# Kernel optimization log

Measured on AMD Instinct MI355X. Metric: run time of the kernel, lower is better.

Reference implementation:

```python
import jax, jax.numpy as jnp
import numpy as np

DIM = 1024
N_HEADS = 16
HEAD_DIM = DIM // N_HEADS
B, N, M = 2, 2048, 2048


def setup_inputs() -> dict:
    key = jax.random.key(0)
    ks = jax.random.split(key, 10)
    s = 1.0 / np.sqrt(DIM)
    return {
        "x1": jax.random.normal(ks[0], (B, N, DIM), dtype=jnp.float32),
        "x2": jax.random.normal(ks[1], (B, M, DIM), dtype=jnp.float32),
        "Wq": jax.random.normal(ks[2], (DIM, DIM), dtype=jnp.float32) * s,
        "bq": jnp.zeros((DIM,), dtype=jnp.float32),
        "Wk": jax.random.normal(ks[3], (DIM, DIM), dtype=jnp.float32) * s,
        "bk": jnp.zeros((DIM,), dtype=jnp.float32),
        "Wv": jax.random.normal(ks[4], (DIM, DIM), dtype=jnp.float32) * s,
        "bv": jnp.zeros((DIM,), dtype=jnp.float32),
        "Wo": jax.random.normal(ks[5], (DIM, DIM), dtype=jnp.float32) * s,
        "bo": jnp.zeros((DIM,), dtype=jnp.float32),
    }


def reference(x1, x2, Wq, bq, Wk, bk, Wv, bv, Wo, bo):
    b, n, _ = x1.shape
    m = x2.shape[1]
    # projections (Linear: x @ W^T + b)
    q = x1 @ Wq.T + bq  # [b, n, dim]
    k = x2 @ Wk.T + bk  # [b, m, dim]
    v = x2 @ Wv.T + bv  # [b, m, dim]
    # split heads -> [b, h, seq, head_dim]
    q = q.reshape(b, n, N_HEADS, HEAD_DIM).transpose(0, 2, 1, 3)
    k = k.reshape(b, m, N_HEADS, HEAD_DIM).transpose(0, 2, 1, 3)
    v = v.reshape(b, m, N_HEADS, HEAD_DIM).transpose(0, 2, 1, 3)
    scale = 1.0 / jnp.sqrt(jnp.asarray(HEAD_DIM, dtype=q.dtype))
    scores = jnp.einsum('bhnd,bhmd->bhnm', q, k) * scale  # [b, h, n, m]
    attn = jax.nn.softmax(scores, axis=-1)
    o = jnp.einsum('bhnm,bhmd->bhnd', attn, v)  # [b, h, n, head_dim]
    o = o.transpose(0, 2, 1, 3).reshape(b, n, DIM)  # merge heads
    return o @ Wo.T + bo
```

## Files before the change

### kernel.cpp

```cpp
#include <hip/hip_runtime.h>
#include <stdint.h>

typedef unsigned short u16;
typedef __attribute__((ext_vector_type(4))) float f32x4;
typedef __attribute__((ext_vector_type(16))) float f32x16;
typedef __attribute__((ext_vector_type(8))) __bf16 bf16x8;
typedef __attribute__((ext_vector_type(8))) unsigned short u16x8;
typedef __attribute__((ext_vector_type(4))) unsigned short u16x4;

#define DIM_    1024
#define NHEADS_ 16
#define HD_     64
#define BB_     2
#define NN_     2048
#define MM_     2048

#define QSCALE 0.180336884f

__device__ inline u16 f32_to_bf16u(float f) {
  union { float f; uint32_t u; } x; x.f = f;
  uint32_t r = x.u + 0x7FFFu + ((x.u >> 16) & 1u);
  return (u16)(r >> 16);
}

__device__ inline void gload_lds16(const u16* g, u16* l) {
  u16* gnc = const_cast<u16*>(g);
  __builtin_amdgcn_global_load_lds(
      (__attribute__((address_space(1))) void*)gnc,
      (__attribute__((address_space(3))) void*)l, 16, 0, 0);
}

__device__ inline uint32_t cvt_pk_bf16(float lo, float hi) {
  uint32_t r;
  asm("v_cvt_pk_bf16_f32 %0, %1, %2" : "=v"(r) : "v"(lo), "v"(hi));
  return r;
}
__device__ inline void permlane32_swap(uint32_t& a, uint32_t& b) {
  asm("v_permlane32_swap_b32 %0, %1" : "+v"(a), "+v"(b));
}

__global__ void cast_all(const float* s0, u16* d0, const float* s1, u16* d1,
                         const float* s2, u16* d2, const float* s3, u16* d3,
                         const float* s4, u16* d4, const float* s5, u16* d5) {
  const float* s; u16* d; int n4;
  switch (blockIdx.y) {
    case 0: s = s0; d = d0; n4 = (BB_ * NN_ * DIM_) / 4; break;
    case 1: s = s1; d = d1; n4 = (BB_ * MM_ * DIM_) / 4; break;
    case 2: s = s2; d = d2; n4 = (DIM_ * DIM_) / 4; break;
    case 3: s = s3; d = d3; n4 = (DIM_ * DIM_) / 4; break;
    case 4: s = s4; d = d4; n4 = (DIM_ * DIM_) / 4; break;
    default: s = s5; d = d5; n4 = (DIM_ * DIM_) / 4; break;
  }
  int stride = gridDim.x * blockDim.x;
  for (int i = blockIdx.x * blockDim.x + threadIdx.x; i < n4; i += stride) {
    float4 f = reinterpret_cast<const float4*>(s)[i];
    u16x4 u;
    u.x = f32_to_bf16u(f.x);
    u.y = f32_to_bf16u(f.y);
    u.z = f32_to_bf16u(f.z);
    u.w = f32_to_bf16u(f.w);
    reinterpret_cast<u16x4*>(d)[i] = u;
  }
}

#define BM 128
#define BN 128
#define BK 64

template <bool BF16OUT>
__device__ __forceinline__
void gemm_body(const u16* __restrict__ A, const u16* __restrict__ Bm,
               const float* __restrict__ bias, void* __restrict__ Cout,
               int M, int N, int K, float scale,
               u16* As , u16* Bs ) {
  const int tid  = threadIdx.x;
  const int lane = tid & 63;
  const int wid  = tid >> 6;
  const int wr = wid >> 2, wc = wid & 3;
  const int fr = lane & 15, fq = lane >> 4;
  const int bm = blockIdx.x, bn = blockIdx.y;
  const int lrow = lane >> 3;
  const int scol = (((lane & 7) ^ lrow) * 8);

  f32x4 acc[4][2];
  #pragma unroll
  for (int m = 0; m < 4; ++m)
    #pragma unroll
    for (int n = 0; n < 2; ++n)
      acc[m][n] = f32x4{0.f, 0.f, 0.f, 0.f};

  const int NT = K / BK;

  auto stage = [&](int buf, int t) {
    int k0 = t * BK;
    #pragma unroll
    for (int c = 0; c < 2; ++c) {
      int ch  = wid * 2 + c;
      int row = ch * 8 + lrow;
      gload_lds16(A  + (size_t)(bm * BM + row) * K + k0 + scol, &As[buf * BM * BK + ch * 512]);
      gload_lds16(Bm + (size_t)(bn * BN + row) * K + k0 + scol, &Bs[buf * BN * BK + ch * 512]);
    }
  };

  stage(0, 0);
  __syncthreads();
  int cur = 0;
  for (int t = 0; t < NT; ++t) {
    if (t + 1 < NT) stage(cur ^ 1, t + 1);
    #pragma unroll
    for (int ks = 0; ks < 2; ++ks) {
      bf16x8 af[4], bfr[2];
      #pragma unroll
      for (int m = 0; m < 4; ++m)
        af[m] = *reinterpret_cast<const bf16x8*>(
            &As[cur * BM * BK + (wr * 64 + m * 16 + fr) * BK + (((ks * 4 + fq) ^ (fr & 7)) * 8)]);
      #pragma unroll
      for (int n = 0; n < 2; ++n)
        bfr[n] = *reinterpret_cast<const bf16x8*>(
            &Bs[cur * BN * BK + (wc * 32 + n * 16 + fr) * BK + (((ks * 4 + fq) ^ (fr & 7)) * 8)]);
      __builtin_amdgcn_s_setprio(1);
      #pragma unroll
      for (int m = 0; m < 4; ++m)
        #pragma unroll
        for (int n = 0; n < 2; ++n)
          acc[m][n] = __builtin_amdgcn_mfma_f32_16x16x32_bf16(af[m], bfr[n], acc[m][n], 0, 0, 0);
      __builtin_amdgcn_s_setprio(0);
    }
    __syncthreads();
    cur ^= 1;
  }

  #pragma unroll
  for (int n = 0; n < 2; ++n) {
    int col = bn * BN + wc * 32 + n * 16 + fr;
    float bv = bias[col];
    #pragma unroll
    for (int m = 0; m < 4; ++m) {
      #pragma unroll
      for (int i = 0; i < 4; ++i) {
        int row = bm * BM + wr * 64 + m * 16 + fq * 4 + i;
        float v = (acc[m][n][i] + bv) * scale;
        if (BF16OUT)
          ((u16*)Cout)[(size_t)row * N + col] = f32_to_bf16u(v);
        else
          ((float*)Cout)[(size_t)row * N + col] = v;
      }
    }
  }
}

__global__ __launch_bounds__(512)
void gemm_qkv(const u16* __restrict__ x1b, const u16* __restrict__ x2b,
              const u16* __restrict__ Wqb, const float* __restrict__ bq, u16* qb,
              const u16* __restrict__ Wkb, const float* __restrict__ bk, u16* kb,
              const u16* __restrict__ Wvb, const float* __restrict__ bv, u16* vb) {
  __shared__ __align__(16) u16 As[2 * BM * BK];
  __shared__ __align__(16) u16 Bs[2 * BN * BK];
  const u16* A; const u16* W; const float* bias; u16* C; float scale;
  switch (blockIdx.z) {
    case 0:  A = x1b; W = Wqb; bias = bq; C = qb; scale = QSCALE; break;
    case 1:  A = x2b; W = Wkb; bias = bk; C = kb; scale = 1.0f;   break;
    default: A = x2b; W = Wvb; bias = bv; C = vb; scale = 1.0f;   break;
  }
  gemm_body<true>(A, W, bias, C, BB_ * NN_, DIM_, DIM_, scale, As, Bs);
}

__global__ __launch_bounds__(512)
void gemm_o(const u16* __restrict__ A, const u16* __restrict__ W,
            const float* __restrict__ bias, float* __restrict__ C) {
  __shared__ __align__(16) u16 As[2 * BM * BK];
  __shared__ __align__(16) u16 Bs[2 * BN * BK];
  gemm_body<false>(A, W, bias, C, BB_ * NN_, DIM_, DIM_, 1.0f, As, Bs);
}

#define QB 128
#define KVB 64

__global__ __launch_bounds__(512)
void attn_fwd(const u16* __restrict__ qg, const u16* __restrict__ kg,
              const u16* __restrict__ vg, u16* __restrict__ og) {
  __shared__ __align__(16) u16 KVs[6 * KVB * HD_];
  const int tid = threadIdx.x, lane = tid & 63, wid = tid >> 6;
  const int hi = lane >> 5;
  const int l31 = lane & 31;
  const int wq = wid >> 1, wk = wid & 1;

  int lin = blockIdx.x + gridDim.x * (blockIdx.y + gridDim.y * blockIdx.z);
  int xcd = lin & 7, slot = lin >> 3;
  int r = slot & 15, gg2 = slot >> 4;
  int g = xcd + 8 * gg2;
  int h = g & 15, b = g >> 4;

  const size_t base_q  = (size_t)b * NN_ * DIM_ + (size_t)h * HD_;
  const size_t base_kv = (size_t)b * MM_ * DIM_ + (size_t)h * HD_;
  const int lrow = lane >> 3;
  const int scol = (((lane & 7) ^ lrow) * 8);

  bf16x8 qf[4];
  const int qrow = r * QB + wq * 32 + l31;
  #pragma unroll
  for (int step = 0; step < 4; ++step)
    qf[step] = *reinterpret_cast<const bf16x8*>(
        qg + base_q + (size_t)qrow * DIM_ + step * 16 + hi * 8);

  bf16x8 onesf;
  #pragma unroll
  for (int j = 0; j < 8; ++j) onesf[j] = (__bf16)1.0f;

  f32x16 oacc[2];
  #pragma unroll
  for (int dgrp = 0; dgrp < 2; ++dgrp)
    #pragma unroll
    for (int rg = 0; rg < 16; ++rg) oacc[dgrp][rg] = 0.f;
  f32x16 lacc;
  #pragma unroll
  for (int rg = 0; rg < 16; ++rg) lacc[rg] = 0.f;

  const int NT = MM_ / KVB;

  auto stageK = [&](int buf, int t) {
    int kv0 = t * KVB;
    int row = wid * 8 + lrow;
    gload_lds16(kg + base_kv + (size_t)(kv0 + row) * DIM_ + scol,
                &KVs[buf * 4096 + wid * 512]);
  };
  auto loadV = [&](int t, u16x8& vpre) {
    int kv0 = t * KVB;
    vpre = *reinterpret_cast<const u16x8*>(vg + base_kv + (size_t)(kv0 + lane) * DIM_ + wid * 8);
  };
  auto writeVT = [&](int buf, const u16x8& vpre) {
    #pragma unroll
    for (int j = 0; j < 8; ++j)
      KVs[(3 + buf) * 4096 + (wid * 8 + j) * KVB + (((lane >> 3) ^ j) * 8) + (lane & 7)] = vpre[j];
  };

  union PB { uint32_t w[4]; bf16x8 v; };

  auto compute = [&](int buf) {
    const u16* Kb = &KVs[buf * 4096];
    const u16* Vb = &KVs[(3 + buf) * 4096];
    f32x16 s;
    #pragma unroll
    for (int rg = 0; rg < 16; ++rg) s[rg] = 0.f;
    __builtin_amdgcn_s_setprio(1);
    #pragma unroll
    for (int step = 0; step < 4; ++step) {
      bf16x8 kf = *reinterpret_cast<const bf16x8*>(
          (const char*)Kb + (wk * 32 + l31) * 128 + (((step * 2 + hi) ^ (lane & 7)) * 16));
      s = __builtin_amdgcn_mfma_f32_32x32x16_bf16(kf, qf[step], s, 0, 0, 0);
    }
    __builtin_amdgcn_s_setprio(0);

    float p[16];
    #pragma unroll
    for (int rg = 0; rg < 16; ++rg) p[rg] = __builtin_amdgcn_exp2f(s[rg]);

    PB pb[2];
    #pragma unroll
    for (int u = 0; u < 2; ++u) {
      uint32_t x0 = cvt_pk_bf16(p[u * 8 + 0], p[u * 8 + 1]);
      uint32_t y0 = cvt_pk_bf16(p[u * 8 + 4], p[u * 8 + 5]);
      permlane32_swap(x0, y0);
      uint32_t x1 = cvt_pk_bf16(p[u * 8 + 2], p[u * 8 + 3]);
      uint32_t y1 = cvt_pk_bf16(p[u * 8 + 6], p[u * 8 + 7]);
      permlane32_swap(x1, y1);
      pb[u].w[0] = x0; pb[u].w[1] = x1; pb[u].w[2] = y0; pb[u].w[3] = y1;
    }

    __builtin_amdgcn_s_setprio(1);
    #pragma unroll
    for (int u = 0; u < 2; ++u)
      lacc = __builtin_amdgcn_mfma_f32_32x32x16_bf16(onesf, pb[u].v, lacc, 0, 0, 0);
    #pragma unroll
    for (int dgrp = 0; dgrp < 2; ++dgrp)
      #pragma unroll
      for (int u = 0; u < 2; ++u) {
        bf16x8 vf = *reinterpret_cast<const bf16x8*>(
            (const char*)Vb + (dgrp * 32 + l31) * 128 +
            (((wk * 4 + u * 2 + hi) ^ (lane & 7)) * 16));
        oacc[dgrp] = __builtin_amdgcn_mfma_f32_32x32x16_bf16(vf, pb[u].v, oacc[dgrp], 0, 0, 0);
      }
    __builtin_amdgcn_s_setprio(0);
  };

  {
    u16x8 v0, v1;
    loadV(0, v0);
    loadV(1, v1);
    stageK(0, 0);
    stageK(1, 1);
    writeVT(0, v0);
    writeVT(1, v1);
    __syncthreads();
  }

  int cur = 0, stg = 2;
  for (int t = 0; t < NT; ++t) {
    u16x8 vpre;
    bool pre = (t + 2 < NT);
    if (pre) {
      loadV(t + 2, vpre);
      stageK(stg, t + 2);
    }
    compute(cur);
    if (pre) writeVT(stg, vpre);
    __syncthreads();
    cur = (cur == 2) ? 0 : cur + 1;
    stg = (stg == 2) ? 0 : stg + 1;
  }

  float* Od = (float*)&KVs[0];
  float* Ls = (float*)&KVs[0] + 128 * 65;
  u16*  Of  = (u16*)&KVs[0];

  if (wk == 1) {
    #pragma unroll
    for (int dgrp = 0; dgrp < 2; ++dgrp)
      #pragma unroll
      for (int rg = 0; rg < 16; ++rg) {
        int d = dgrp * 32 + (rg & 3) + 8 * (rg >> 2) + 4 * hi;
        Od[(wq * 32 + l31) * 65 + d] = oacc[dgrp][rg];
      }
    if (hi == 0) Ls[wq * 32 + l31] = lacc[0];
  }
  __syncthreads();
  if (wk == 0) {
    float inv = 1.f / (lacc[0] + Ls[wq * 32 + l31]);
    #pragma unroll
    for (int dgrp = 0; dgrp < 2; ++dgrp)
      #pragma unroll
      for (int rg = 0; rg < 16; ++rg) {
        int d = dgrp * 32 + (rg & 3) + 8 * (rg >> 2) + 4 * hi;
        oacc[dgrp][rg] = (oacc[dgrp][rg] + Od[(wq * 32 + l31) * 65 + d]) * inv;
      }
  }
  __syncthreads();
  if (wk == 0) {
    #pragma unroll
    for (int dgrp = 0; dgrp < 2; ++dgrp)
      #pragma unroll
      for (int rg = 0; rg < 16; ++rg) {
        int d = dgrp * 32 + (rg & 3) + 8 * (rg >> 2) + 4 * hi;
        Of[(wq * 32 + l31) * 68 + d] = f32_to_bf16u(oacc[dgrp][rg]);
      }
  }
  __syncthreads();
  #pragma unroll
  for (int itr = 0; itr < 2; ++itr) {
    int idx = itr * 512 + tid;
    int qq = idx >> 3;
    int ck = idx & 7;
    u16x8 v = *reinterpret_cast<const u16x8*>(&Of[qq * 68 + ck * 8]);
    *reinterpret_cast<u16x8*>(og + base_q + (size_t)(r * QB + qq) * DIM_ + ck * 8) = v;
  }
}

extern "C" void kernel_launch(void* const* d_in, const int* in_sizes, int n_in,
                              void* d_out, int out_size, void* d_ws, size_t ws_size,
                              hipStream_t stream) {
  (void)in_sizes; (void)n_in; (void)out_size; (void)ws_size;
  const float* x1 = (const float*)d_in[0];
  const float* x2 = (const float*)d_in[1];
  const float* Wq = (const float*)d_in[2];
  const float* bq = (const float*)d_in[3];
  const float* Wk = (const float*)d_in[4];
  const float* bk = (const float*)d_in[5];
  const float* Wv = (const float*)d_in[6];
  const float* bv = (const float*)d_in[7];
  const float* Wo = (const float*)d_in[8];
  const float* bo = (const float*)d_in[9];
  float* out = (float*)d_out;

  char* ws = (char*)d_ws;
  u16* x1b = (u16*)(ws);
  u16* x2b = (u16*)(ws + (8u  << 20));
  u16* Wqb = (u16*)(ws + (16u << 20));
  u16* Wkb = (u16*)(ws + (18u << 20));
  u16* Wvb = (u16*)(ws + (20u << 20));
  u16* Wob = (u16*)(ws + (22u << 20));
  u16* qb  = (u16*)(ws + (24u << 20));
  u16* kb  = (u16*)(ws + (32u << 20));
  u16* vb  = (u16*)(ws + (40u << 20));
  u16* ob  = (u16*)(ws + (48u << 20));

  cast_all<<<dim3(512, 6), 256, 0, stream>>>(x1, x1b, x2, x2b, Wq, Wqb,
                                             Wk, Wkb, Wv, Wvb, Wo, Wob);

  const int Mrows = BB_ * NN_;
  dim3 gqkv(Mrows / BM, DIM_ / BN, 3);
  gemm_qkv<<<gqkv, 512, 0, stream>>>(x1b, x2b, Wqb, bq, qb, Wkb, bk, kb, Wvb, bv, vb);

  dim3 ga(NN_ / QB, NHEADS_, BB_);
  attn_fwd<<<ga, 512, 0, stream>>>(qb, kb, vb, ob);

  dim3 gg(Mrows / BM, DIM_ / BN);
  gemm_o<<<gg, 512, 0, stream>>>(ob, Wob, bo, out);
}
```

Baseline: 117.2 us.

## Halve attention block to 4 waves with 64 query rows per wave

The attention kernel now launches 256 threads per block, and each wave handles two 32-row query fragments. Each K fragment read from LDS feeds two MFMAs and each V fragment feeds two, which halves LDS traffic per MFMA. The row sum is now accumulated with scalar VALU adds plus a cross-half shuffle instead of the ones-matrix MFMA. In exchange, register pressure roughly doubles for the accumulators and Q fragments, and per-thread staging work for K and V doubles, which may reduce occupancy.

Result: slower. 124.4 us (+6.1%).

```diff
diff --git a/kernel.cpp b/kernel.cpp
--- a/kernel.cpp
+++ b/kernel.cpp
@@ -176,7 +176,7 @@
 #define QB 128
 #define KVB 64
 
-__global__ __launch_bounds__(512)
+__global__ __launch_bounds__(256)
 void attn_fwd(const u16* __restrict__ qg, const u16* __restrict__ kg,
               const u16* __restrict__ vg, u16* __restrict__ og) {
   __shared__ __align__(16) u16 KVs[6 * KVB * HD_];
@@ -196,42 +196,51 @@
   const int lrow = lane >> 3;
   const int scol = (((lane & 7) ^ lrow) * 8);
 
-  bf16x8 qf[4];
-  const int qrow = r * QB + wq * 32 + l31;
-  #pragma unroll
-  for (int step = 0; step < 4; ++step)
-    qf[step] = *reinterpret_cast<const bf16x8*>(
-        qg + base_q + (size_t)qrow * DIM_ + step * 16 + hi * 8);
-
-  bf16x8 onesf;
-  #pragma unroll
-  for (int j = 0; j < 8; ++j) onesf[j] = (__bf16)1.0f;
-
-  f32x16 oacc[2];
-  #pragma unroll
-  for (int dgrp = 0; dgrp < 2; ++dgrp)
-    #pragma unroll
-    for (int rg = 0; rg < 16; ++rg) oacc[dgrp][rg] = 0.f;
-  f32x16 lacc;
-  #pragma unroll
-  for (int rg = 0; rg < 16; ++rg) lacc[rg] = 0.f;
+  bf16x8 qfr[2][4];
+  const int qbase = r * QB + wq * 64;
+  #pragma unroll
+  for (int qf = 0; qf < 2; ++qf)
+    #pragma unroll
+    for (int step = 0; step < 4; ++step)
+      qfr[qf][step] = *reinterpret_cast<const bf16x8*>(
+          qg + base_q + (size_t)(qbase + qf * 32 + l31) * DIM_ + step * 16 + hi * 8);
+
+  f32x16 oacc[2][2];
+  #pragma unroll
+  for (int qf = 0; qf < 2; ++qf)
+    #pragma unroll
+    for (int dgrp = 0; dgrp < 2; ++dgrp)
+      #pragma unroll
+      for (int rg = 0; rg < 16; ++rg) oacc[qf][dgrp][rg] = 0.f;
+  float l_run[2] = {0.f, 0.f};
 
   const int NT = MM_ / KVB;
 
   auto stageK = [&](int buf, int t) {
     int kv0 = t * KVB;
-    int row = wid * 8 + lrow;
-    gload_lds16(kg + base_kv + (size_t)(kv0 + row) * DIM_ + scol,
-                &KVs[buf * 4096 + wid * 512]);
+    #pragma unroll
+    for (int c = 0; c < 2; ++c) {
+      int ch = wid * 2 + c;
+      int row = ch * 8 + lrow;
+      gload_lds16(kg + base_kv + (size_t)(kv0 + row) * DIM_ + scol,
+                  &KVs[buf * 4096 + ch * 512]);
+    }
   };
-  auto loadV = [&](int t, u16x8& vpre) {
+  auto loadV = [&](int t, u16x8* vpre) {
     int kv0 = t * KVB;
-    vpre = *reinterpret_cast<const u16x8*>(vg + base_kv + (size_t)(kv0 + lane) * DIM_ + wid * 8);
+    #pragma unroll
+    for (int p = 0; p < 2; ++p)
+      vpre[p] = *reinterpret_cast<const u16x8*>(
+          vg + base_kv + (size_t)(kv0 + lane) * DIM_ + (wid * 2 + p) * 8);
   };
-  auto writeVT = [&](int buf, const u16x8& vpre) {
-    #pragma unroll
-    for (int j = 0; j < 8; ++j)
-      KVs[(3 + buf) * 4096 + (wid * 8 + j) * KVB + (((lane >> 3) ^ j) * 8) + (lane & 7)] = vpre[j];
+  auto writeVT = [&](int buf, const u16x8* vpre) {
+    #pragma unroll
+    for (int p = 0; p < 2; ++p) {
+      int c = wid * 2 + p;
+      #pragma unroll
+      for (int j = 0; j < 8; ++j)
+        KVs[(3 + buf) * 4096 + (c * 8 + j) * KVB + (((lane >> 3) ^ j) * 8) + (lane & 7)] = vpre[p][j];
+    }
   };
 
   union PB { uint32_t w[4]; bf16x8 v; };
@@ -239,38 +248,44 @@
   auto compute = [&](int buf) {
     const u16* Kb = &KVs[buf * 4096];
     const u16* Vb = &KVs[(3 + buf) * 4096];
-    f32x16 s;
-    #pragma unroll
-    for (int rg = 0; rg < 16; ++rg) s[rg] = 0.f;
+    f32x16 s[2];
+    #pragma unroll
+    for (int qf = 0; qf < 2; ++qf)
+      #pragma unroll
+      for (int rg = 0; rg < 16; ++rg) s[qf][rg] = 0.f;
     __builtin_amdgcn_s_setprio(1);
     #pragma unroll
     for (int step = 0; step < 4; ++step) {
       bf16x8 kf = *reinterpret_cast<const bf16x8*>(
           (const char*)Kb + (wk * 32 + l31) * 128 + (((step * 2 + hi) ^ (lane & 7)) * 16));
-      s = __builtin_amdgcn_mfma_f32_32x32x16_bf16(kf, qf[step], s, 0, 0, 0);
+      s[0] = __builtin_amdgcn_mfma_f32_32x32x16_bf16(kf, qfr[0][step], s[0], 0, 0, 0);
+      s[1] = __builtin_amdgcn_mfma_f32_32x32x16_bf16(kf, qfr[1][step], s[1], 0, 0, 0);
     }
     __builtin_amdgcn_s_setprio(0);
 
-    float p[16];
-    #pragma unroll
-    for (int rg = 0; rg < 16; ++rg) p[rg] = __builtin_amdgcn_exp2f(s[rg]);
-
-    PB pb[2];
-    #pragma unroll
-    for (int u = 0; u < 2; ++u) {
-      uint32_t x0 = cvt_pk_bf16(p[u * 8 + 0], p[u * 8 + 1]);
-      uint32_t y0 = cvt_pk_bf16(p[u * 8 + 4], p[u * 8 + 5]);
-      permlane32_swap(x0, y0);
-      uint32_t x1 = cvt_pk_bf16(p[u * 8 + 2], p[u * 8 + 3]);
-      uint32_t y1 = cvt_pk_bf16(p[u * 8 + 6], p[u * 8 + 7]);
-      permlane32_swap(x1, y1);
-      pb[u].w[0] = x0; pb[u].w[1] = x1; pb[u].w[2] = y0; pb[u].w[3] = y1;
+    PB pb[2][2];
+    #pragma unroll
+    for (int qf = 0; qf < 2; ++qf) {
+      float p[16];
+      #pragma unroll
+      for (int rg = 0; rg < 16; ++rg) p[rg] = __builtin_amdgcn_exp2f(s[qf][rg]);
+      float lp = 0.f;
+      #pragma unroll
+      for (int rg = 0; rg < 16; ++rg) lp += p[rg];
+      l_run[qf] += lp;
+      #pragma unroll
+      for (int u = 0; u < 2; ++u) {
+        uint32_t x0 = cvt_pk_bf16(p[u * 8 + 0], p[u * 8 + 1]);
+        uint32_t y0 = cvt_pk_bf16(p[u * 8 + 4], p[u * 8 + 5]);
+        permlane32_swap(x0, y0);
+        uint32_t x1 = cvt_pk_bf16(p[u * 8 + 2], p[u * 8 + 3]);
+        uint32_t y1 = cvt_pk_bf16(p[u * 8 + 6], p[u * 8 + 7]);
+        permlane32_swap(x1, y1);
+        pb[qf][u].w[0] = x0; pb[qf][u].w[1] = x1; pb[qf][u].w[2] = y0; pb[qf][u].w[3] = y1;
+      }
     }
 
     __builtin_amdgcn_s_setprio(1);
-    #pragma unroll
-    for (int u = 0; u < 2; ++u)
-      lacc = __builtin_amdgcn_mfma_f32_32x32x16_bf16(onesf, pb[u].v, lacc, 0, 0, 0);
     #pragma unroll
     for (int dgrp = 0; dgrp < 2; ++dgrp)
       #pragma unroll
@@ -278,13 +293,14 @@
         bf16x8 vf = *reinterpret_cast<const bf16x8*>(
             (const char*)Vb + (dgrp * 32 + l31) * 128 +
             (((wk * 4 + u * 2 + hi) ^ (lane & 7)) * 16));
-        oacc[dgrp] = __builtin_amdgcn_mfma_f32_32x32x16_bf16(vf, pb[u].v, oacc[dgrp], 0, 0, 0);
+        oacc[0][dgrp] = __builtin_amdgcn_mfma_f32_32x32x16_bf16(vf, pb[0][u].v, oacc[0][dgrp], 0, 0, 0);
+        oacc[1][dgrp] = __builtin_amdgcn_mfma_f32_32x32x16_bf16(vf, pb[1][u].v, oacc[1][dgrp], 0, 0, 0);
       }
     __builtin_amdgcn_s_setprio(0);
   };
 
   {
-    u16x8 v0, v1;
+    u16x8 v0[2], v1[2];
     loadV(0, v0);
     loadV(1, v1);
     stageK(0, 0);
@@ -296,7 +312,7 @@
 
   int cur = 0, stg = 2;
   for (int t = 0; t < NT; ++t) {
-    u16x8 vpre;
+    u16x8 vpre[2];
     bool pre = (t + 2 < NT);
     if (pre) {
       loadV(t + 2, vpre);
@@ -313,41 +329,58 @@
   float* Ls = (float*)&KVs[0] + 128 * 65;
   u16*  Of  = (u16*)&KVs[0];
 
+  float lh[2];
+  #pragma unroll
+  for (int qf = 0; qf < 2; ++qf)
+    lh[qf] = l_run[qf] + __shfl_xor(l_run[qf], 32, 64);
+
   if (wk == 1) {
     #pragma unroll
-    for (int dgrp = 0; dgrp < 2; ++dgrp)
-      #pragma unroll
-      for (int rg = 0; rg < 16; ++rg) {
-        int d = dgrp * 32 + (rg & 3) + 8 * (rg >> 2) + 4 * hi;
-        Od[(wq * 32 + l31) * 65 + d] = oacc[dgrp][rg];
-      }
-    if (hi == 0) Ls[wq * 32 + l31] = lacc[0];
+    for (int qf = 0; qf < 2; ++qf) {
+      int q = wq * 64 + qf * 32 + l31;
+      #pragma unroll
+      for (int dgrp = 0; dgrp < 2; ++dgrp)
+        #pragma unroll
+        for (int rg = 0; rg < 16; ++rg) {
+          int d = dgrp * 32 + (rg & 3) + 8 * (rg >> 2) + 4 * hi;
+          Od[q * 65 + d] = oacc[qf][dgrp][rg];
+        }
+      if (hi == 0) Ls[q] = lh[qf];
+    }
   }
   __syncthreads();
   if (wk == 0) {
-    float inv = 1.f / (lacc[0] + Ls[wq * 32 + l31]);
-    #pragma unroll
-    for (int dgrp = 0; dgrp < 2; ++dgrp)
-      #pragma unroll
-      for (int rg = 0; rg < 16; ++rg) {
-        int d = dgrp * 32 + (rg & 3) + 8 * (rg >> 2) + 4 * hi;
-        oacc[dgrp][rg] = (oacc[dgrp][rg] + Od[(wq * 32 + l31) * 65 + d]) * inv;
-      }
+    #pragma unroll
+    for (int qf = 0; qf < 2; ++qf) {
+      int q = wq * 64 + qf * 32 + l31;
+      float inv = 1.f / (lh[qf] + Ls[q]);
+      #pragma unroll
+      for (int dgrp = 0; dgrp < 2; ++dgrp)
+        #pragma unroll
+        for (int rg = 0; rg < 16; ++rg) {
+          int d = dgrp * 32 + (rg & 3) + 8 * (rg >> 2) + 4 * hi;
+          oacc[qf][dgrp][rg] = (oacc[qf][dgrp][rg] + Od[q * 65 + d]) * inv;
+        }
+    }
   }
   __syncthreads();
   if (wk == 0) {
     #pragma unroll
-    for (int dgrp = 0; dgrp < 2; ++dgrp)
-      #pragma unroll
-      for (int rg = 0; rg < 16; ++rg) {
-        int d = dgrp * 32 + (rg & 3) + 8 * (rg >> 2) + 4 * hi;
-        Of[(wq * 32 + l31) * 68 + d] = f32_to_bf16u(oacc[dgrp][rg]);
-      }
+    for (int qf = 0; qf < 2; ++qf) {
+      int q = wq * 64 + qf * 32 + l31;
+      #pragma unroll
+      for (int dgrp = 0; dgrp < 2; ++dgrp)
+        #pragma unroll
+        for (int rg = 0; rg < 16; ++rg) {
+          int d = dgrp * 32 + (rg & 3) + 8 * (rg >> 2) + 4 * hi;
+          Of[q * 68 + d] = f32_to_bf16u(oacc[qf][dgrp][rg]);
+        }
+    }
   }
   __syncthreads();
   #pragma unroll
-  for (int itr = 0; itr < 2; ++itr) {
-    int idx = itr * 512 + tid;
+  for (int itr = 0; itr < 4; ++itr) {
+    int idx = itr * 256 + tid;
     int qq = idx >> 3;
     int ck = idx & 7;
     u16x8 v = *reinterpret_cast<const u16x8*>(&Of[qq * 68 + ck * 8]);
@@ -391,7 +424,7 @@
   gemm_qkv<<<gqkv, 512, 0, stream>>>(x1b, x2b, Wqb, bq, qb, Wkb, bk, kb, Wvb, bv, vb);
 
   dim3 ga(NN_ / QB, NHEADS_, BB_);
-  attn_fwd<<<ga, 512, 0, stream>>>(qb, kb, vb, ob);
+  attn_fwd<<<ga, 256, 0, stream>>>(qb, kb, vb, ob);
 
   dim3 gg(Mrows / BM, DIM_ / BN);
   gemm_o<<<gg, 512, 0, stream>>>(ob, Wob, bo, out);
```
